# Performance work log

Measured on AMD Instinct MI355X. Metric: run time of the kernel, lower is better.

## Reference

```python
import jax, jax.numpy as jnp
import numpy as np

B, T, C, H = 8, 1024, 1024, 16
D = C // H
EPS = 1e-5


def setup_inputs() -> dict:
    key = jax.random.key(0)
    ks = jax.random.split(key, 12)
    s = lambda k, shape, scale=0.02: jax.random.normal(k, shape, dtype=jnp.float32) * scale
    return {
        "x": jax.random.normal(ks[0], (B, T, C), dtype=jnp.float32),
        "ln1_w": jnp.ones((C,), jnp.float32),
        "ln1_b": jnp.zeros((C,), jnp.float32),
        "w_qkv": s(ks[1], (C, 3 * C)),
        "b_qkv": jnp.zeros((3 * C,), jnp.float32),
        "w_o": s(ks[2], (C, C)),
        "b_o": jnp.zeros((C,), jnp.float32),
        "ln2_w": jnp.ones((C,), jnp.float32),
        "ln2_b": jnp.zeros((C,), jnp.float32),
        "w_fc": s(ks[3], (C, 4 * C)),
        "b_fc": jnp.zeros((4 * C,), jnp.float32),
        "w_proj": s(ks[4], (4 * C, C)),
        "b_proj": jnp.zeros((C,), jnp.float32),
    }


def _layernorm(x, w, b):
    mu = jnp.mean(x, axis=-1, keepdims=True)
    var = jnp.mean(jnp.square(x - mu), axis=-1, keepdims=True)
    return (x - mu) * jax.lax.rsqrt(var + EPS) * w + b


def _attention(x, w_qkv, b_qkv, w_o, b_o):
    b, t, c = x.shape
    qkv = x @ w_qkv + b_qkv                      # [B,T,3C]
    q, k, v = jnp.split(qkv, 3, axis=-1)
    q = q.reshape(b, t, H, D)
    k = k.reshape(b, t, H, D)
    v = v.reshape(b, t, H, D)
    scores = jnp.einsum("bqhd,bkhd->bhqk", q, k) / jnp.sqrt(jnp.float32(D))
    mask = jnp.tril(jnp.ones((t, t), dtype=bool))  # causal
    scores = jnp.where(mask, scores, jnp.float32(-jnp.inf))
    att = jax.nn.softmax(scores, axis=-1)
    y = jnp.einsum("bhqk,bkhd->bqhd", att, v).reshape(b, t, c)
    return y @ w_o + b_o


def _mlp(x, w_fc, b_fc, w_proj, b_proj):
    h = jax.nn.gelu(x @ w_fc + b_fc, approximate=True)  # tanh GELU
    return h @ w_proj + b_proj


def reference(x, ln1_w, ln1_b, w_qkv, b_qkv, w_o, b_o, ln2_w, ln2_b, w_fc, b_fc, w_proj, b_proj):
    x = x + _attention(_layernorm(x, ln1_w, ln1_b), w_qkv, b_qkv, w_o, b_o)
    x = x + _mlp(_layernorm(x, ln2_w, ln2_b), w_fc, b_fc, w_proj, b_proj)
    return x
```

## Files before the change

### kernel.cpp

```cpp
#include <hip/hip_runtime.h>
#include <math.h>
#include <stdint.h>

typedef unsigned short u16;
typedef unsigned int u32;
typedef __attribute__((ext_vector_type(4))) unsigned short u16x4;
typedef __attribute__((ext_vector_type(8))) unsigned short u16x8;
typedef __attribute__((ext_vector_type(8))) __bf16 bf16x8;
typedef __attribute__((ext_vector_type(4))) float f32x4;

#define Bn 8
#define Tn 1024
#define Cn 1024
#define Hn 16
#define Dn 64
#define Mn 8192

#define F32_ONE_BITS 0x3F800000u

__device__ __forceinline__ float b2f(u16 u) {
  union { unsigned int i; float f; } v; v.i = ((unsigned int)u) << 16; return v.f;
}
__device__ __forceinline__ u16 f2b(float f) {
  union { float f; unsigned int i; } v; v.f = f;
  unsigned int r = v.i + 0x7fffu + ((v.i >> 16) & 1u);
  return (u16)(r >> 16);
}

__device__ __forceinline__ void async_ld16(const u16* g, u16* l) {
  __builtin_amdgcn_global_load_lds(
      (__attribute__((address_space(1))) void*)g,
      (__attribute__((address_space(3))) void*)l, 16, 0, 0);
}

template <int N> __device__ __forceinline__ void wait_vmcnt() {
  if constexpr (N == 8)      asm volatile("s_waitcnt vmcnt(8)" ::: "memory");
  else if constexpr (N == 6) asm volatile("s_waitcnt vmcnt(6)" ::: "memory");
  else if constexpr (N == 4) asm volatile("s_waitcnt vmcnt(4)" ::: "memory");
  else                       asm volatile("s_waitcnt vmcnt(0)" ::: "memory");
}
__device__ __forceinline__ void raw_barrier() {
  asm volatile("s_barrier" ::: "memory");
}

__device__ __forceinline__ float gelu_fast(float x) {
  float u2 = 1.5957691216057308f * (x + 0.044715f * x * x * x);
  return x / (1.0f + __expf(-u2));
}

__global__ __launch_bounds__(256) void cvt_x_k(const void* __restrict__ src, u16* __restrict__ dst,
                                               const u32* __restrict__ flagp) {
  bool isf32 = (*flagp == F32_ONE_BITS);
  size_t i = ((size_t)blockIdx.x * 256 + threadIdx.x) * 4;
  if (isf32) {
    f32x4 v = *reinterpret_cast<const f32x4*>((const float*)src + i);
    u16x4 o;
#pragma unroll
    for (int j = 0; j < 4; j++) o[j] = f2b(v[j]);
    *reinterpret_cast<u16x4*>(dst + i) = o;
  } else {
    *reinterpret_cast<u16x4*>(dst + i) = *reinterpret_cast<const u16x4*>((const u16*)src + i);
  }
}

struct SmallCvt { const void* src[8]; u16* dst[8]; int n[8]; };

__global__ __launch_bounds__(256) void cvt_small_k(SmallCvt p, const u32* __restrict__ flagp) {
  bool isf32 = (*flagp == F32_ONE_BITS);
  int t = blockIdx.x * 256 + threadIdx.x;
  int off = 0;
#pragma unroll
  for (int i = 0; i < 8; i++) {
    int idx = t - off;
    if (idx >= 0 && idx < p.n[i]) {
      u16 v = isf32 ? f2b(((const float*)p.src[i])[idx]) : ((const u16*)p.src[i])[idx];
      p.dst[i][idx] = v;
    }
    off += p.n[i];
  }
}

__global__ __launch_bounds__(256) void transpose_k(const void* __restrict__ in,
                                                   u16* __restrict__ out, int K, int N,
                                                   const u32* __restrict__ flagp) {
  bool isf32 = (*flagp == F32_ONE_BITS);
  __shared__ u16 tile[32][33];
  int c0 = blockIdx.x * 32, r0 = blockIdx.y * 32;
  int tx = threadIdx.x, ty = threadIdx.y;
#pragma unroll
  for (int i = 0; i < 4; i++) {
    size_t idx = (size_t)(r0 + ty + i * 8) * N + c0 + tx;
    tile[ty + i * 8][tx] = isf32 ? f2b(((const float*)in)[idx]) : ((const u16*)in)[idx];
  }
  __syncthreads();
#pragma unroll
  for (int i = 0; i < 4; i++)
    out[(size_t)(c0 + ty + i * 8) * K + r0 + tx] = tile[tx][ty + i * 8];
}

__global__ __launch_bounds__(256) void ln_k(const u16* __restrict__ x, const u16* __restrict__ w,
                                            const u16* __restrict__ bi, u16* __restrict__ out) {
  int row = blockIdx.x, tid = threadIdx.x;
  const u16* xr = x + (size_t)row * Cn;
  u16x4 xv = *reinterpret_cast<const u16x4*>(xr + tid * 4);
  float v0 = b2f(xv[0]), v1 = b2f(xv[1]), v2 = b2f(xv[2]), v3 = b2f(xv[3]);
  float s = v0 + v1 + v2 + v3;
  float s2 = v0 * v0 + v1 * v1 + v2 * v2 + v3 * v3;
#pragma unroll
  for (int m = 1; m < 64; m <<= 1) {
    s += __shfl_xor(s, m, 64);
    s2 += __shfl_xor(s2, m, 64);
  }
  __shared__ float rs_[4], rs2_[4];
  int wave = tid >> 6, lane = tid & 63;
  if (lane == 0) { rs_[wave] = s; rs2_[wave] = s2; }
  __syncthreads();
  s = rs_[0] + rs_[1] + rs_[2] + rs_[3];
  s2 = rs2_[0] + rs2_[1] + rs2_[2] + rs2_[3];
  float mu = s * (1.0f / Cn);
  float var = s2 * (1.0f / Cn) - mu * mu;
  float rstd = rsqrtf(var + 1e-5f);
  u16x4 wv = *reinterpret_cast<const u16x4*>(w + tid * 4);
  u16x4 bv = *reinterpret_cast<const u16x4*>(bi + tid * 4);
  u16x4 ov;
  float vv[4] = {v0, v1, v2, v3};
#pragma unroll
  for (int j = 0; j < 4; j++)
    ov[j] = f2b((vv[j] - mu) * rstd * b2f(wv[j]) + b2f(bv[j]));
  *reinterpret_cast<u16x4*>(out + (size_t)row * Cn + tid * 4) = ov;
}

template <int BN_T, int GELU, int RES, int F32OUT>
__global__ __launch_bounds__(512, 2) void gemm3_k(const u16* __restrict__ A, const u16* __restrict__ BT,
                                                  const u16* __restrict__ bias, const u16* __restrict__ res,
                                                  void* __restrict__ Cout, int M, int N, int K) {
  constexpr int NI = BN_T / 64;
  constexpr int NB = NI;
  constexpr int AE = 256 * 64;
  constexpr int BE = BN_T * 64;

  __shared__ __align__(16) u16 As[2 * AE];
  __shared__ __align__(16) u16 Bs[2 * BE];

  int tid = threadIdx.x, wave = tid >> 6, lane = tid & 63;
  int l15 = lane & 15, quad = lane >> 4;

  int nbx = gridDim.x;
  int nwg = nbx * gridDim.y;
  int lin = blockIdx.y * nbx + blockIdx.x;
  int cpx = nwg >> 3;
  int swz = (lin & 7) * cpx + (lin >> 3);
  int m0 = (swz / nbx) * 256;
  int n0 = (swz % nbx) * BN_T;

  int wm = (wave >> 2) * 128;
  int wn = (wave & 3) * (NI * 16);

  int offA0, offA1, offB0, offB1;
  {
    int x0 = ((0 + quad) ^ (l15 & 7)) * 8;
    int x1 = ((4 + quad) ^ (l15 & 7)) * 8;
    offA0 = (wm + l15) * 64 + x0;
    offA1 = (wm + l15) * 64 + x1;
    offB0 = (wn + l15) * 64 + x0;
    offB1 = (wn + l15) * 64 + x1;
  }

  const u16* aS[4]; int aD[4];
#pragma unroll
  for (int i = 0; i < 4; i++) {
    int c = i * 512 + tid;
    int row = c >> 3, j = (c & 7) ^ (row & 7);
    aS[i] = A + (size_t)(m0 + row) * K + j * 8;
    aD[i] = c * 8;
  }
  const u16* bS[NB]; int bD[NB];
#pragma unroll
  for (int i = 0; i < NB; i++) {
    int c = i * 512 + tid;
    int row = c >> 3, j = (c & 7) ^ (row & 7);
    bS[i] = BT + (size_t)(n0 + row) * K + j * 8;
    bD[i] = c * 8;
  }

#define ISSA(T, I) async_ld16(aS[I] + (size_t)(T) * 64, &As[((T) & 1) * AE + aD[I]])
#define ISSB(T, I) async_ld16(bS[I] + (size_t)(T) * 64, &Bs[((T) & 1) * BE + bD[I]])
#define LDF(P) (*reinterpret_cast<const bf16x8*>(P))
#define MM(AV, BV, CC) CC = __builtin_amdgcn_mfma_f32_16x16x32_bf16(AV, BV, CC, 0, 0, 0)

  f32x4 acc[8][NI];
#pragma unroll
  for (int mi = 0; mi < 8; mi++)
#pragma unroll
    for (int ni = 0; ni < NI; ni++) acc[mi][ni] = (f32x4){0.f, 0.f, 0.f, 0.f};

  int NT = K >> 6;

#pragma unroll
  for (int i = 0; i < 4; i++) ISSA(0, i);
#pragma unroll
  for (int i = 0; i < NB; i++) ISSB(0, i);
#pragma unroll
  for (int i = 0; i < 4; i++) ISSA(1, i);
#pragma unroll
  for (int i = 0; i < NB; i++) ISSB(1, i);
  wait_vmcnt<4 + NB>();
  raw_barrier();

  bf16x8 bv[NI][2];

#pragma unroll 2
  for (int t = 0; t < NT; ++t) {
    const u16* Ab = &As[(t & 1) * AE];
    const u16* Bb = &Bs[(t & 1) * BE];
    bool haveN = (t >= 1) && (t + 1 < NT);
    bool haveNN = (t + 2 < NT);

    {
      bf16x8 a0 = LDF(Ab + offA0);
      bf16x8 a1 = LDF(Ab + offA0 + 1024);
      bf16x8 a2 = LDF(Ab + offA0 + 2048);
      bf16x8 a3 = LDF(Ab + offA0 + 3072);
#pragma unroll
      for (int ni = 0; ni < NI; ni++) bv[ni][0] = LDF(Bb + offB0 + ni * 1024);
      if (haveN) ISSA(t + 1, 1);
      raw_barrier();
      __builtin_amdgcn_s_setprio(1);
#pragma unroll
      for (int ni = 0; ni < NI; ni++) {
        MM(a0, bv[ni][0], acc[0][ni]);
        MM(a1, bv[ni][0], acc[1][ni]);
        MM(a2, bv[ni][0], acc[2][ni]);
        MM(a3, bv[ni][0], acc[3][ni]);
      }
      __builtin_amdgcn_s_setprio(0);
      raw_barrier();
    }
    {
      bf16x8 a0 = LDF(Ab + offA1);
      bf16x8 a1 = LDF(Ab + offA1 + 1024);
      bf16x8 a2 = LDF(Ab + offA1 + 2048);
      bf16x8 a3 = LDF(Ab + offA1 + 3072);
#pragma unroll
      for (int ni = 0; ni < NI; ni++) bv[ni][1] = LDF(Bb + offB1 + ni * 1024);
      if (haveN) ISSA(t + 1, 3);
      raw_barrier();
      __builtin_amdgcn_s_setprio(1);
#pragma unroll
      for (int ni = 0; ni < NI; ni++) {
        MM(a0, bv[ni][1], acc[0][ni]);
        MM(a1, bv[ni][1], acc[1][ni]);
        MM(a2, bv[ni][1], acc[2][ni]);
        MM(a3, bv[ni][1], acc[3][ni]);
      }
      __builtin_amdgcn_s_setprio(0);
      raw_barrier();
    }
    {
      bf16x8 a0 = LDF(Ab + offA0 + 4096);
      bf16x8 a1 = LDF(Ab + offA0 + 5120);
      bf16x8 a2 = LDF(Ab + offA0 + 6144);
      bf16x8 a3 = LDF(Ab + offA0 + 7168);
      if (haveNN) {
        ISSA(t + 2, 0);
        ISSB(t + 2, 0);
        if constexpr (NB == 4) ISSB(t + 2, 1);
      }
      raw_barrier();
      __builtin_amdgcn_s_setprio(1);
#pragma unroll
      for (int ni = 0; ni < NI; ni++) {
        MM(a0, bv[ni][0], acc[4][ni]);
        MM(a1, bv[ni][0], acc[5][ni]);
        MM(a2, bv[ni][0], acc[6][ni]);
        MM(a3, bv[ni][0], acc[7][ni]);
      }
      __builtin_amdgcn_s_setprio(0);
      raw_barrier();
    }
    {
      bf16x8 a0 = LDF(Ab + offA1 + 4096);
      bf16x8 a1 = LDF(Ab + offA1 + 5120);
      bf16x8 a2 = LDF(Ab + offA1 + 6144);
      bf16x8 a3 = LDF(Ab + offA1 + 7168);
      if (haveNN) {
        ISSA(t + 2, 2);
        if constexpr (NB == 4) { ISSB(t + 2, 2); ISSB(t + 2, 3); }
        else ISSB(t + 2, 1);
      }
      raw_barrier();
      __builtin_amdgcn_s_setprio(1);
#pragma unroll
      for (int ni = 0; ni < NI; ni++) {
        MM(a0, bv[ni][1], acc[4][ni]);
        MM(a1, bv[ni][1], acc[5][ni]);
        MM(a2, bv[ni][1], acc[6][ni]);
        MM(a3, bv[ni][1], acc[7][ni]);
      }
      __builtin_amdgcn_s_setprio(0);
      if (haveNN) wait_vmcnt<2 + NB>();
      else wait_vmcnt<0>();
      raw_barrier();
    }
  }
#undef ISSA
#undef ISSB
#undef LDF
#undef MM

#pragma unroll
  for (int ni = 0; ni < NI; ni++) {
    int col = n0 + wn + ni * 16 + l15;
    float bval = b2f(bias[col]);
#pragma unroll
    for (int mi = 0; mi < 8; mi++) {
#pragma unroll
      for (int r = 0; r < 4; r++) {
        int row = m0 + wm + mi * 16 + quad * 4 + r;
        float v = acc[mi][ni][r] + bval;
        if (GELU) v = gelu_fast(v);
        if (RES) v += b2f(res[(size_t)row * N + col]);
        if (F32OUT)
          ((float*)Cout)[(size_t)row * N + col] = v;
        else
          ((u16*)Cout)[(size_t)row * N + col] = f2b(v);
      }
    }
  }
}

#define ATTN_PROC(QF, O, M_R, L_R, Q0, KV0, KSB)                                      \
  do {                                                                                \
    float sv[4][4];                                                                   \
    _Pragma("unroll")                                                                 \
    for (int ni = 0; ni < 4; ni++) {                                                  \
      f32x4 z = (f32x4){0.f, 0.f, 0.f, 0.f};                                          \
      _Pragma("unroll")                                                               \
      for (int kc = 0; kc < 2; kc++) {                                                \
        bf16x8 bfr = *reinterpret_cast<const bf16x8*>((KSB) + offKb[kc] + ni * 1024); \
        z = __builtin_amdgcn_mfma_f32_16x16x32_bf16(QF[kc], bfr, z, 0, 0, 0);         \
      }                                                                               \
      _Pragma("unroll")                                                               \
      for (int r = 0; r < 4; r++) sv[ni][r] = z[r];                                   \
    }                                                                                 \
    bool diag = ((KV0) + 64 > (Q0));                                                  \
    _Pragma("unroll")                                                                 \
    for (int ni = 0; ni < 4; ni++)                                                    \
      _Pragma("unroll")                                                               \
      for (int r = 0; r < 4; r++) {                                                   \
        float v = sv[ni][r] * 0.125f;                                                 \
        if (diag && ((KV0) + ni * 16 + l15 > (Q0) + quad * 4 + r)) v = -1e30f;        \
        sv[ni][r] = v;                                                                \
      }                                                                               \
    float mt[4], al[4], rs[4];                                                        \
    _Pragma("unroll")                                                                 \
    for (int r = 0; r < 4; r++) {                                                     \
      mt[r] = fmaxf(fmaxf(sv[0][r], sv[1][r]), fmaxf(sv[2][r], sv[3][r]));            \
      _Pragma("unroll")                                                               \
      for (int m = 1; m <= 8; m <<= 1) mt[r] = fmaxf(mt[r], __shfl_xor(mt[r], m, 64));\
      float mn = fmaxf(M_R[r], mt[r]);                                                \
      al[r] = __expf(M_R[r] - mn);                                                    \
      M_R[r] = mn;                                                                    \
      rs[r] = 0.f;                                                                    \
    }                                                                                 \
    _Pragma("unroll")                                                                 \
    for (int ni = 0; ni < 4; ni++)                                                    \
      _Pragma("unroll")                                                               \
      for (int r = 0; r < 4; r++) {                                                   \
        float p = __expf(sv[ni][r] - M_R[r]);                                         \
        sv[ni][r] = p;                                                                \
        rs[r] += p;                                                                   \
      }                                                                               \
    _Pragma("unroll")                                                                 \
    for (int r = 0; r < 4; r++) {                                                     \
      _Pragma("unroll")                                                               \
      for (int m = 1; m <= 8; m <<= 1) rs[r] += __shfl_xor(rs[r], m, 64);             \
      L_R[r] = L_R[r] * al[r] + rs[r];                                                \
    }                                                                                 \
    _Pragma("unroll")                                                                 \
    for (int dn = 0; dn < 4; dn++)                                                    \
      _Pragma("unroll")                                                               \
      for (int r = 0; r < 4; r++) O[dn][r] *= al[r];                                  \
    _Pragma("unroll")                                                                 \
    for (int ni = 0; ni < 4; ni++)                                                    \
      _Pragma("unroll")                                                               \
      for (int r = 0; r < 4; r++)                                                     \
        Ps[wave][pwBase + r * 72 + ni * 16] = f2b(sv[ni][r]);                         \
    _Pragma("unroll")                                                                 \
    for (int kc = 0; kc < 2; kc++) {                                                  \
      bf16x8 afr = *reinterpret_cast<const bf16x8*>(&Ps[wave][prBase + kc * 32]);     \
      _Pragma("unroll")                                                               \
      for (int dn = 0; dn < 4; dn++) {                                                \
        bf16x8 bfr = *reinterpret_cast<const bf16x8*>(&VTs[vrBase + dn * 1152 + kc * 32]); \
        O[dn] = __builtin_amdgcn_mfma_f32_16x16x32_bf16(afr, bfr, O[dn], 0, 0, 0);    \
      }                                                                               \
    }                                                                                 \
  } while (0)

__global__ __launch_bounds__(256, 4) void attn_k(const u16* __restrict__ qkv, u16* __restrict__ y) {
  int bh = blockIdx.x;
  int lo = blockIdx.y;
  int hi = 15 - lo;
  int b = bh >> 4, h = bh & 15;
  int tid = threadIdx.x, wave = tid >> 6, lane = tid & 63;
  int l15 = lane & 15, quad = lane >> 4;

  __shared__ __align__(16) u16 Ks[2][64 * 64];
  __shared__ __align__(16) u16 VTs[64 * 72];
  __shared__ __align__(16) u16 Ps[4][16 * 72];

  const u16* base = qkv + (size_t)b * Tn * 3072 + h * 64;
  int q0_lo = lo * 64 + wave * 16;
  int q0_hi = hi * 64 + wave * 16;

  bf16x8 qf_lo[2], qf_hi[2];
#pragma unroll
  for (int kc = 0; kc < 2; kc++) {
    qf_lo[kc] = *reinterpret_cast<const bf16x8*>(base + (size_t)(q0_lo + l15) * 3072 + kc * 32 + quad * 8);
    qf_hi[kc] = *reinterpret_cast<const bf16x8*>(base + (size_t)(q0_hi + l15) * 3072 + kc * 32 + quad * 8);
  }

  int offKb[2];
#pragma unroll
  for (int kc = 0; kc < 2; kc++)
    offKb[kc] = l15 * 64 + (((kc * 4 + quad) ^ (l15 & 7)) * 8);

  int kSrcOff[2], kDstOff[2];
#pragma unroll
  for (int i = 0; i < 2; i++) {
    int c = wave * 128 + i * 64 + lane;
    int row = c >> 3, j = (c & 7) ^ (row & 7);
    kSrcOff[i] = row * 3072 + j * 8;
    kDstOff[i] = c * 8;
  }
  const u16* kBase = base + 1024;
  const u16* vBase = base + 2048;
  int kp = tid & 31, dgroup = tid >> 5;
  u32* vtw = reinterpret_cast<u32*>(VTs);

#pragma unroll
  for (int i = 0; i < 2; i++) async_ld16(kBase + kSrcOff[i], &Ks[0][kDstOff[i]]);
  u16x8 va, vb;
  {
    const u16* vS = vBase + (size_t)(2 * kp) * 3072 + dgroup * 8;
    va = *reinterpret_cast<const u16x8*>(vS);
    vb = *reinterpret_cast<const u16x8*>(vS + 3072);
  }

  f32x4 o_lo[4], o_hi[4];
  float m_lo[4], l_lo[4], m_hi[4], l_hi[4];
#pragma unroll
  for (int i = 0; i < 4; i++) {
    o_lo[i] = (f32x4){0.f, 0.f, 0.f, 0.f};
    o_hi[i] = (f32x4){0.f, 0.f, 0.f, 0.f};
    m_lo[i] = -1e30f; m_hi[i] = -1e30f;
    l_lo[i] = 0.f;    l_hi[i] = 0.f;
  }

  int pwBase = quad * 4 * 72 + l15;
  int prBase = l15 * 72 + quad * 8;
  int vrBase = l15 * 72 + quad * 8;

  int kvend_hi = hi * 64, kvend_lo = lo * 64;
  int buf = 0;
  for (int kv0 = 0; kv0 <= kvend_hi; kv0 += 64) {
    __syncthreads();
#pragma unroll
    for (int i = 0; i < 8; i++)
      vtw[(dgroup * 8 + i) * 36 + kp] = (u32)va[i] | ((u32)vb[i] << 16);
    __syncthreads();
    if (kv0 + 64 <= kvend_hi) {
      const u16* kS = kBase + (size_t)(kv0 + 64) * 3072;
#pragma unroll
      for (int i = 0; i < 2; i++) async_ld16(kS + kSrcOff[i], &Ks[buf ^ 1][kDstOff[i]]);
      const u16* vS = vBase + (size_t)(kv0 + 64 + 2 * kp) * 3072 + dgroup * 8;
      va = *reinterpret_cast<const u16x8*>(vS);
      vb = *reinterpret_cast<const u16x8*>(vS + 3072);
    }
    {
      const u16* KsB = &Ks[buf][0];
      ATTN_PROC(qf_hi, o_hi, m_hi, l_hi, q0_hi, kv0, KsB);
      if (kv0 <= kvend_lo)
        ATTN_PROC(qf_lo, o_lo, m_lo, l_lo, q0_lo, kv0, KsB);
    }
    buf ^= 1;
  }

#pragma unroll
  for (int r = 0; r < 4; r++) {
    float inv = 1.0f / l_hi[r];
    int row = b * Tn + q0_hi + quad * 4 + r;
#pragma unroll
    for (int dn = 0; dn < 4; dn++)
      y[(size_t)row * Cn + h * 64 + dn * 16 + l15] = f2b(o_hi[dn][r] * inv);
  }
#pragma unroll
  for (int r = 0; r < 4; r++) {
    float inv = 1.0f / l_lo[r];
    int row = b * Tn + q0_lo + quad * 4 + r;
#pragma unroll
    for (int dn = 0; dn < 4; dn++)
      y[(size_t)row * Cn + h * 64 + dn * 16 + l15] = f2b(o_lo[dn][r] * inv);
  }
}

extern "C" void kernel_launch(void* const* d_in, const int* in_sizes, int n_in,
                              void* d_out, int out_size, void* d_ws, size_t ws_size,
                              hipStream_t stream) {
  const void* x      = d_in[0];
  const void* ln1_w  = d_in[1];
  const void* ln1_b  = d_in[2];
  const void* w_qkv  = d_in[3];
  const void* b_qkv  = d_in[4];
  const void* w_o    = d_in[5];
  const void* b_o    = d_in[6];
  const void* ln2_w  = d_in[7];
  const void* ln2_b  = d_in[8];
  const void* w_fc   = d_in[9];
  const void* b_fc   = d_in[10];
  const void* w_proj = d_in[11];
  const void* b_proj = d_in[12];
  const u32* flagp = (const u32*)ln1_w;

  size_t off = 0;
  char* wsb = (char*)d_ws;
  auto alloc = [&](size_t bytes) {
    void* p = wsb + off;
    off += (bytes + 255) & ~(size_t)255;
    return (u16*)p;
  };
  u16* wqkvT  = alloc((size_t)3072 * 1024 * 2);
  u16* woT    = alloc((size_t)1024 * 1024 * 2);
  u16* wfcT   = alloc((size_t)4096 * 1024 * 2);
  u16* wprojT = alloc((size_t)1024 * 4096 * 2);
  u16* xb     = alloc((size_t)Mn * 1024 * 2);
  u16* sm     = alloc((size_t)16384 * 2);
  u16* xn     = alloc((size_t)Mn * 1024 * 2);
  u16* ybuf   = alloc((size_t)Mn * 1024 * 2);
  u16* x1     = alloc((size_t)Mn * 1024 * 2);
  u16* big    = alloc((size_t)Mn * 4096 * 2);
  u16* qkvbuf = big;
  u16* hbuf   = big;
  if (off > ws_size) return;

  u16* LW1 = sm;
  u16* LB1 = sm + 1024;
  u16* BQKV = sm + 2048;
  u16* BO  = sm + 5120;
  u16* LW2 = sm + 6144;
  u16* LB2 = sm + 7168;
  u16* BFC = sm + 8192;
  u16* BPJ = sm + 12288;

  SmallCvt sc;
  sc.src[0] = ln1_w;  sc.dst[0] = LW1;  sc.n[0] = 1024;
  sc.src[1] = ln1_b;  sc.dst[1] = LB1;  sc.n[1] = 1024;
  sc.src[2] = b_qkv;  sc.dst[2] = BQKV; sc.n[2] = 3072;
  sc.src[3] = b_o;    sc.dst[3] = BO;   sc.n[3] = 1024;
  sc.src[4] = ln2_w;  sc.dst[4] = LW2;  sc.n[4] = 1024;
  sc.src[5] = ln2_b;  sc.dst[5] = LB2;  sc.n[5] = 1024;
  sc.src[6] = b_fc;   sc.dst[6] = BFC;  sc.n[6] = 4096;
  sc.src[7] = b_proj; sc.dst[7] = BPJ;  sc.n[7] = 1024;

  hipLaunchKernelGGL(cvt_small_k, dim3(52), dim3(256), 0, stream, sc, flagp);
  hipLaunchKernelGGL(cvt_x_k, dim3(Mn * 1024 / 4 / 256), dim3(256), 0, stream, x, xb, flagp);

  dim3 tb(32, 8);
  hipLaunchKernelGGL(transpose_k, dim3(3072 / 32, 1024 / 32), tb, 0, stream, w_qkv, wqkvT, 1024, 3072, flagp);
  hipLaunchKernelGGL(transpose_k, dim3(1024 / 32, 1024 / 32), tb, 0, stream, w_o, woT, 1024, 1024, flagp);
  hipLaunchKernelGGL(transpose_k, dim3(4096 / 32, 1024 / 32), tb, 0, stream, w_fc, wfcT, 1024, 4096, flagp);
  hipLaunchKernelGGL(transpose_k, dim3(1024 / 32, 4096 / 32), tb, 0, stream, w_proj, wprojT, 4096, 1024, flagp);

  hipLaunchKernelGGL(ln_k, dim3(Mn), dim3(256), 0, stream, xb, LW1, LB1, xn);
  hipLaunchKernelGGL((gemm3_k<256, 0, 0, 0>), dim3(3072 / 256, Mn / 256), dim3(512), 0, stream,
                     xn, wqkvT, BQKV, (const u16*)nullptr, (void*)qkvbuf, Mn, 3072, 1024);
  hipLaunchKernelGGL(attn_k, dim3(Bn * Hn, 8), dim3(256), 0, stream, qkvbuf, ybuf);
  hipLaunchKernelGGL((gemm3_k<128, 0, 1, 0>), dim3(1024 / 128, Mn / 256), dim3(512), 0, stream,
                     ybuf, woT, BO, xb, (void*)x1, Mn, 1024, 1024);
  hipLaunchKernelGGL(ln_k, dim3(Mn), dim3(256), 0, stream, x1, LW2, LB2, xn);
  hipLaunchKernelGGL((gemm3_k<256, 1, 0, 0>), dim3(4096 / 256, Mn / 256), dim3(512), 0, stream,
                     xn, wfcT, BFC, (const u16*)nullptr, (void*)hbuf, Mn, 4096, 1024);
  hipLaunchKernelGGL((gemm3_k<128, 0, 1, 1>), dim3(1024 / 128, Mn / 256), dim3(512), 0, stream,
                     hbuf, wprojT, BPJ, x1, d_out, Mn, 1024, 4096);
}
```

Baseline: 547.5 us.

## Add quadrant-phased 256x256 GEMM and simple 128x128 GEMM for projections

```diff
diff --git a/kernel.cpp b/kernel.cpp
--- a/kernel.cpp
+++ b/kernel.cpp
@@ -128,6 +128,236 @@
   for (int j = 0; j < 4; j++)
     ov[j] = f2b((vv[j] - mu) * rstd * b2f(wv[j]) + b2f(bv[j]));
   *reinterpret_cast<u16x4*>(out + (size_t)row * Cn + tid * 4) = ov;
+}
+
+template <int GELU, int RES, int F32OUT>
+__global__ __launch_bounds__(512, 2) void gemm5_k(const u16* __restrict__ A, const u16* __restrict__ BT,
+                                                  const u16* __restrict__ bias, const u16* __restrict__ res,
+                                                  void* __restrict__ Cout, int M, int N, int K) {
+  __shared__ __align__(16) u16 As[4 * 128 * 64];
+  __shared__ __align__(16) u16 Bs[4 * 128 * 64];
+
+  int tid = threadIdx.x, wave = tid >> 6, lane = tid & 63;
+  int l15 = lane & 15, quad = lane >> 4;
+
+  int nbx = gridDim.x;
+  int nwg = nbx * gridDim.y;
+  int lin = blockIdx.y * nbx + blockIdx.x;
+  int cpx = nwg >> 3;
+  int swz = (lin & 7) * cpx + (lin >> 3);
+  int m0 = (swz / nbx) * 256;
+  int n0 = (swz % nbx) * 256;
+
+  int wqm = (wave >> 2) * 64;
+  int wqn = (wave & 3) * 32;
+
+  int offA[2], offB[2];
+#pragma unroll
+  for (int kc = 0; kc < 2; kc++) {
+    int x = ((kc * 4 + quad) ^ (l15 & 7)) * 8;
+    offA[kc] = (wqm + l15) * 64 + x;
+    offB[kc] = (wqn + l15) * 64 + x;
+  }
+
+  const u16* aSrc[2][2];
+  const u16* bSrc[2][2];
+  int stD[2];
+#pragma unroll
+  for (int i = 0; i < 2; i++) {
+    int c = i * 512 + tid;
+    int row = c >> 3, j = (c & 7) ^ (row & 7);
+    stD[i] = c * 8;
+    aSrc[0][i] = A + (size_t)(m0 + row) * K + j * 8;
+    aSrc[1][i] = A + (size_t)(m0 + 128 + row) * K + j * 8;
+    bSrc[0][i] = BT + (size_t)(n0 + row) * K + j * 8;
+    bSrc[1][i] = BT + (size_t)(n0 + 128 + row) * K + j * 8;
+  }
+
+#define STG_A(T, MH)                                                              \
+  do {                                                                            \
+    _Pragma("unroll")                                                             \
+    for (int i_ = 0; i_ < 2; i_++)                                                \
+      async_ld16(aSrc[MH][i_] + (size_t)(T) * 64,                                 \
+                 &As[((MH) * 2 + ((T) & 1)) * 8192 + stD[i_]]);                   \
+  } while (0)
+#define STG_B(T, NH)                                                              \
+  do {                                                                            \
+    _Pragma("unroll")                                                             \
+    for (int i_ = 0; i_ < 2; i_++)                                                \
+      async_ld16(bSrc[NH][i_] + (size_t)(T) * 64,                                 \
+                 &Bs[((NH) * 2 + ((T) & 1)) * 8192 + stD[i_]]);                   \
+  } while (0)
+#define MMQ(AV, BV, CC) CC = __builtin_amdgcn_mfma_f32_16x16x32_bf16(AV, BV, CC, 0, 0, 0)
+
+#define QPHASE(MH, NH, DO_RA, DO_RB, AB, BB, STGSTMT)                             \
+  do {                                                                            \
+    if (DO_RA) {                                                                  \
+      _Pragma("unroll")                                                           \
+      for (int mi = 0; mi < 4; mi++)                                              \
+        _Pragma("unroll")                                                         \
+        for (int kc = 0; kc < 2; kc++)                                            \
+          aF[mi][kc] = *reinterpret_cast<const bf16x8*>((AB) + offA[kc] + mi * 1024); \
+    }                                                                             \
+    if (DO_RB) {                                                                  \
+      _Pragma("unroll")                                                           \
+      for (int ni = 0; ni < 2; ni++)                                              \
+        _Pragma("unroll")                                                         \
+        for (int kc = 0; kc < 2; kc++)                                            \
+          bF[ni][kc] = *reinterpret_cast<const bf16x8*>((BB) + offB[kc] + ni * 1024); \
+    }                                                                             \
+    STGSTMT;                                                                      \
+    raw_barrier();                                                                \
+    __builtin_amdgcn_s_setprio(1);                                                \
+    _Pragma("unroll")                                                             \
+    for (int mi = 0; mi < 4; mi++)                                                \
+      _Pragma("unroll")                                                           \
+      for (int ni = 0; ni < 2; ni++) {                                            \
+        MMQ(aF[mi][0], bF[ni][0], acc[(MH) * 4 + mi][(NH) * 2 + ni]);             \
+        MMQ(aF[mi][1], bF[ni][1], acc[(MH) * 4 + mi][(NH) * 2 + ni]);             \
+      }                                                                           \
+    __builtin_amdgcn_s_setprio(0);                                                \
+    if (st) wait_vmcnt<4>(); else wait_vmcnt<0>();                                \
+    raw_barrier();                                                                \
+  } while (0)
+
+  f32x4 acc[8][4];
+#pragma unroll
+  for (int i = 0; i < 8; i++)
+#pragma unroll
+    for (int j = 0; j < 4; j++) acc[i][j] = (f32x4){0.f, 0.f, 0.f, 0.f};
+
+  int NT = K >> 6;
+
+  STG_A(0, 0);
+  STG_B(0, 0);
+  STG_B(0, 1);
+  STG_A(0, 1);
+  wait_vmcnt<4>();
+  raw_barrier();
+
+  bf16x8 aF[4][2], bF[2][2];
+
+  for (int t = 0; t < NT; ++t) {
+    const u16* A0p = &As[(t & 1) * 8192];
+    const u16* A1p = &As[(2 + (t & 1)) * 8192];
+    const u16* B0p = &Bs[(t & 1) * 8192];
+    const u16* B1p = &Bs[(2 + (t & 1)) * 8192];
+    bool st = (t + 1 < NT);
+
+    QPHASE(0, 0, true,  true,  A0p, B0p, if (st) STG_A(t + 1, 0));
+    QPHASE(0, 1, false, true,  A0p, B1p, if (st) STG_B(t + 1, 0));
+    QPHASE(1, 1, true,  false, A1p, B1p, if (st) STG_B(t + 1, 1));
+    QPHASE(1, 0, false, true,  A1p, B0p, if (st) STG_A(t + 1, 1));
+  }
+#undef QPHASE
+#undef STG_A
+#undef STG_B
+#undef MMQ
+
+#pragma unroll
+  for (int j = 0; j < 4; j++) {
+    int col = n0 + (j >> 1) * 128 + wqn + (j & 1) * 16 + l15;
+    float bval = b2f(bias[col]);
+#pragma unroll
+    for (int i = 0; i < 8; i++) {
+#pragma unroll
+      for (int r = 0; r < 4; r++) {
+        int row = m0 + (i >> 2) * 128 + wqm + (i & 3) * 16 + quad * 4 + r;
+        float v = acc[i][j][r] + bval;
+        if (GELU) v = gelu_fast(v);
+        if (RES) v += b2f(res[(size_t)row * N + col]);
+        if (F32OUT)
+          ((float*)Cout)[(size_t)row * N + col] = v;
+        else
+          ((u16*)Cout)[(size_t)row * N + col] = f2b(v);
+      }
+    }
+  }
+}
+
+template <int GELU, int RES, int F32OUT>
+__global__ __launch_bounds__(256) void gemm_k(const u16* __restrict__ A, const u16* __restrict__ BT,
+                                              const u16* __restrict__ bias, const u16* __restrict__ res,
+                                              void* __restrict__ Cout, int M, int N, int K) {
+  __shared__ __align__(16) u16 As[128 * 64];
+  __shared__ __align__(16) u16 Bs[128 * 64];
+  int tid = threadIdx.x, wave = tid >> 6, lane = tid & 63;
+  int l15 = lane & 15, quad = lane >> 4;
+  int m0 = blockIdx.y * 128, n0 = blockIdx.x * 128;
+  int wm = (wave & 1) * 64, wn = (wave >> 1) * 64;
+
+  int offA[4][2], offB[4][2];
+#pragma unroll
+  for (int i = 0; i < 4; i++) {
+    int rowA = wm + i * 16 + l15;
+    int rowB = wn + i * 16 + l15;
+#pragma unroll
+    for (int kc = 0; kc < 2; kc++) {
+      offA[i][kc] = rowA * 64 + (((kc * 4 + quad) ^ (rowA & 7)) * 8);
+      offB[i][kc] = rowB * 64 + (((kc * 4 + quad) ^ (rowB & 7)) * 8);
+    }
+  }
+
+  const u16 *aSrc[4], *bSrc[4];
+  u16 *aDst[4], *bDst[4];
+#pragma unroll
+  for (int i = 0; i < 4; i++) {
+    int c = wave * 256 + i * 64 + lane;
+    int row = c >> 3;
+    int j = (c & 7) ^ (row & 7);
+    aSrc[i] = A + (size_t)(m0 + row) * K + j * 8;
+    bSrc[i] = BT + (size_t)(n0 + row) * K + j * 8;
+    aDst[i] = As + (size_t)c * 8;
+    bDst[i] = Bs + (size_t)c * 8;
+  }
+
+  f32x4 acc[4][4];
+#pragma unroll
+  for (int mi = 0; mi < 4; mi++)
+#pragma unroll
+    for (int ni = 0; ni < 4; ni++) acc[mi][ni] = (f32x4){0.f, 0.f, 0.f, 0.f};
+
+  for (int k0 = 0; k0 < K; k0 += 64) {
+    __syncthreads();
+#pragma unroll
+    for (int i = 0; i < 4; i++) async_ld16(aSrc[i] + k0, aDst[i]);
+#pragma unroll
+    for (int i = 0; i < 4; i++) async_ld16(bSrc[i] + k0, bDst[i]);
+    __syncthreads();
+#pragma unroll
+    for (int kc = 0; kc < 2; kc++) {
+      bf16x8 av[4], bv[4];
+#pragma unroll
+      for (int i = 0; i < 4; i++) av[i] = *reinterpret_cast<const bf16x8*>(As + offA[i][kc]);
+#pragma unroll
+      for (int i = 0; i < 4; i++) bv[i] = *reinterpret_cast<const bf16x8*>(Bs + offB[i][kc]);
+#pragma unroll
+      for (int mi = 0; mi < 4; mi++)
+#pragma unroll
+        for (int ni = 0; ni < 4; ni++)
+          acc[mi][ni] = __builtin_amdgcn_mfma_f32_16x16x32_bf16(av[mi], bv[ni], acc[mi][ni], 0, 0, 0);
+    }
+  }
+
+#pragma unroll
+  for (int ni = 0; ni < 4; ni++) {
+    int col = n0 + wn + ni * 16 + l15;
+    float bval = b2f(bias[col]);
+#pragma unroll
+    for (int mi = 0; mi < 4; mi++) {
+#pragma unroll
+      for (int r = 0; r < 4; r++) {
+        int row = m0 + wm + mi * 16 + quad * 4 + r;
+        float v = acc[mi][ni][r] + bval;
+        if (GELU) v = gelu_fast(v);
+        if (RES) v += b2f(res[(size_t)row * N + col]);
+        if (F32OUT)
+          ((float*)Cout)[(size_t)row * N + col] = v;
+        else
+          ((u16*)Cout)[(size_t)row * N + col] = f2b(v);
+      }
+    }
+  }
 }
 
 template <int BN_T, int GELU, int RES, int F32OUT>
@@ -572,13 +802,13 @@
   hipLaunchKernelGGL(transpose_k, dim3(1024 / 32, 4096 / 32), tb, 0, stream, w_proj, wprojT, 4096, 1024, flagp);
 
   hipLaunchKernelGGL(ln_k, dim3(Mn), dim3(256), 0, stream, xb, LW1, LB1, xn);
-  hipLaunchKernelGGL((gemm3_k<256, 0, 0, 0>), dim3(3072 / 256, Mn / 256), dim3(512), 0, stream,
+  hipLaunchKernelGGL((gemm5_k<0, 0, 0>), dim3(3072 / 256, Mn / 256), dim3(512), 0, stream,
                      xn, wqkvT, BQKV, (const u16*)nullptr, (void*)qkvbuf, Mn, 3072, 1024);
   hipLaunchKernelGGL(attn_k, dim3(Bn * Hn, 8), dim3(256), 0, stream, qkvbuf, ybuf);
-  hipLaunchKernelGGL((gemm3_k<128, 0, 1, 0>), dim3(1024 / 128, Mn / 256), dim3(512), 0, stream,
+  hipLaunchKernelGGL((gemm_k<0, 1, 0>), dim3(1024 / 128, Mn / 128), dim3(256), 0, stream,
                      ybuf, woT, BO, xb, (void*)x1, Mn, 1024, 1024);
   hipLaunchKernelGGL(ln_k, dim3(Mn), dim3(256), 0, stream, x1, LW2, LB2, xn);
-  hipLaunchKernelGGL((gemm3_k<256, 1, 0, 0>), dim3(4096 / 256, Mn / 256), dim3(512), 0, stream,
+  hipLaunchKernelGGL((gemm5_k<1, 0, 0>), dim3(4096 / 256, Mn / 256), dim3(512), 0, stream,
                      xn, wfcT, BFC, (const u16*)nullptr, (void*)hbuf, Mn, 4096, 1024);
   hipLaunchKernelGGL((gemm3_k<128, 0, 1, 1>), dim3(1024 / 128, Mn / 256), dim3(512), 0, stream,
                      hbuf, wprojT, BPJ, x1, d_out, Mn, 1024, 4096);
```

After: 531.5 us. 1.03x faster.
